# Performance work log

Measured on AMD Instinct MI355X. Metric: run time of the kernel, lower is better.

## Reference

```python
import jax, jax.numpy as jnp
import numpy as np

NEG = -9e8

def _leaky(x):
    return jax.nn.leaky_relu(x, 0.01)

def _gru(x, h, wih, whh, bih, bhh):
    # torch.nn.GRUCell math
    gi = x @ wih.T + bih
    gh = h @ whh.T + bhh
    ir, iz, inn = jnp.split(gi, 3, axis=-1)
    hr, hz, hn = jnp.split(gh, 3, axis=-1)
    r = jax.nn.sigmoid(ir + hr)
    z = jax.nn.sigmoid(iz + hz)
    n = jnp.tanh(inn + r * hn)
    return (1.0 - z) * n + z * h

def _gather(feat, idx):
    # feat [B,S,F], idx [B,S,K] -> [B,S,K,F]; -1 wraps to last row, masked later (same as torch)
    return jax.vmap(lambda f, i: f[i])(feat, idx)

def setup_inputs() -> dict:
    key = jax.random.key(0)
    ks = jax.random.split(key, 32)
    B, S, K, F_in, E, R = 32, 512, 21, 26, 256, 3
    amino_list = jax.random.uniform(ks[0], (B, S, F_in), dtype=jnp.float32)
    idx = jax.random.randint(ks[1], (B, S, K), 0, S, dtype=jnp.int32)
    pad = jax.random.uniform(ks[2], (B, S, K)) < 0.3
    amino_degree_list = jnp.where(pad, jnp.int32(-1), idx)
    # variable sequence lengths for mask
    lens = jax.random.randint(ks[3], (B,), S // 2, S + 1)
    amino_mask = (jnp.arange(S)[None, :] < lens[:, None]).astype(jnp.float32)
    s = 0.05
    d = dict(
        amino_list=amino_list,
        amino_degree_list=amino_degree_list,
        amino_mask=amino_mask,
        emb_W=jax.random.normal(ks[4], (E, F_in)) * s,
        emb_b=jax.random.normal(ks[5], (E,)) * s,
        neigh_W=jax.random.normal(ks[6], (E, F_in)) * s,
        neigh_b=jax.random.normal(ks[7], (E,)) * s,
        align_W=jax.random.normal(ks[8], (R, 1, 2 * E)) * s,
        align_b=jax.random.normal(ks[9], (R, 1)) * s,
        attend_W=jax.random.normal(ks[10], (R, E, E)) * s,
        attend_b=jax.random.normal(ks[11], (R, E)) * s,
        gru_wih=jax.random.normal(ks[12], (R, 3 * E, E)) * s,
        gru_whh=jax.random.normal(ks[13], (R, 3 * E, E)) * s,
        gru_bih=jax.random.normal(ks[14], (R, 3 * E)) * s,
        gru_bhh=jax.random.normal(ks[15], (R, 3 * E)) * s,
        seq_align_W=jax.random.normal(ks[16], (1, 2 * E)) * s,
        seq_align_b=jax.random.normal(ks[17], (1,)) * s,
        seq_attend_W=jax.random.normal(ks[18], (E, E)) * s,
        seq_attend_b=jax.random.normal(ks[19], (E,)) * s,
        sgru_wih=jax.random.normal(ks[20], (3 * E, E)) * s,
        sgru_whh=jax.random.normal(ks[21], (3 * E, E)) * s,
        sgru_bih=jax.random.normal(ks[22], (3 * E,)) * s,
        sgru_bhh=jax.random.normal(ks[23], (3 * E,)) * s,
    )
    return d

RADIUS = 3
T_STEPS = 2

def reference(amino_list, amino_degree_list, amino_mask,
              emb_W, emb_b, neigh_W, neigh_b,
              align_W, align_b, attend_W, attend_b,
              gru_wih, gru_whh, gru_bih, gru_bhh,
              seq_align_W, seq_align_b, seq_attend_W, seq_attend_b,
              sgru_wih, sgru_whh, sgru_bih, sgru_bhh):
    B, S, _ = amino_list.shape
    E = emb_W.shape[0]
    K = amino_degree_list.shape[-1]

    mask3 = amino_mask[:, :, None]                       # [B,S,1]
    amino_feature = _leaky(amino_list @ emb_W.T + emb_b)  # [B,S,E]

    attend_mask = (amino_degree_list != -1).astype(jnp.float32)[..., None]   # [B,S,K,1]
    softmax_mask = jnp.where(amino_degree_list == -1, NEG, 0.0)[..., None]   # [B,S,K,1]

    # first radius step: neighbors from raw one-hot features via neighbor_fc
    neighbor = _gather(amino_list, amino_degree_list)                 # [B,S,K,F_in]
    neighbor_feature = _leaky(neighbor @ neigh_W.T + neigh_b)         # [B,S,K,E]

    h = amino_feature.reshape(B * S, E)
    activated = None
    for d in range(RADIUS):
        if d == 0:
            nbr = neighbor_feature
            cur = amino_feature
        else:
            nbr = _gather(activated, amino_degree_list)               # [B,S,K,E]
            cur = activated
        cur_exp = jnp.broadcast_to(cur[:, :, None, :], (B, S, K, E))
        feat_align = jnp.concatenate([cur_exp, nbr], axis=-1)         # [B,S,K,2E]
        score = _leaky(feat_align @ align_W[d].T + align_b[d]) + softmax_mask
        attw = jax.nn.softmax(score, axis=-2) * attend_mask           # [B,S,K,1]
        nbr_t = nbr @ attend_W[d].T + attend_b[d]                     # [B,S,K,E]
        context = jax.nn.elu(jnp.sum(attw * nbr_t, axis=-2))          # [B,S,E]
        h = _gru(context.reshape(B * S, E), h, gru_wih[d], gru_whh[d], gru_bih[d], gru_bhh[d])
        activated = jax.nn.relu(h.reshape(B, S, E))

    seq_feature = jnp.sum(activated * mask3, axis=-2)                 # [B,E]
    act_mol = jax.nn.relu(seq_feature)
    seq_softmax_mask = jnp.where(mask3 == 0.0, NEG, 0.0)              # [B,S,1]

    act_seq = act_mol
    for _ in range(T_STEPS):
        mol_exp = jnp.broadcast_to(act_mol[:, None, :], (B, S, E))
        sa = jnp.concatenate([mol_exp, activated], axis=-1)           # [B,S,2E]
        score = _leaky(sa @ seq_align_W.T + seq_align_b) + seq_softmax_mask
        w = jax.nn.softmax(score, axis=-2) * mask3                    # [B,S,1]
        feat_t = activated @ seq_attend_W.T + seq_attend_b            # [B,S,E]
        seq_context = jax.nn.elu(jnp.sum(w * feat_t, axis=-2))        # [B,E]
        seq_feature = _gru(seq_context, seq_feature, sgru_wih, sgru_whh, sgru_bih, sgru_bhh)
        act_seq = jax.nn.relu(seq_feature)
    return act_seq
```

## Files before the change

### kernel.cpp

```cpp
#include <hip/hip_runtime.h>
#include <hip/hip_bf16.h>
#include <math.h>


#define NEGC (-9.0e8f)

typedef __attribute__((ext_vector_type(8))) short bf16x8;
typedef __attribute__((ext_vector_type(4))) float f32x4;

__device__ __forceinline__ ushort f2bf(float x) {
    union { float f; unsigned u; } v; v.f = x;
    unsigned r = v.u + 0x7FFF + ((v.u >> 16) & 1);
    return (ushort)(r >> 16);
}
__device__ __forceinline__ float bf2f(ushort u) {
    union { unsigned u; float f; } v; v.u = ((unsigned)u) << 16;
    return v.f;
}
__device__ __forceinline__ float sigm_fast(float x) {
    return 1.f / (1.f + __expf(-x));
}
__device__ __forceinline__ float tanh_fast(float x) {
    return 1.f - 2.f / (__expf(2.f * x) + 1.f);
}
__device__ __forceinline__ float elu_fast(float x) {
    return x > 0.f ? x : (__expf(x) - 1.f);
}

typedef const __attribute__((address_space(1))) void gvoid_t;
typedef __attribute__((address_space(3))) void lvoid_t;

__global__ __launch_bounds__(256) void cvt4_kernel(
    const float* __restrict__ s0, ushort* __restrict__ d0, int n0,
    const float* __restrict__ s1, ushort* __restrict__ d1, int n1,
    const float* __restrict__ s2, ushort* __restrict__ d2, int n2,
    const float* __restrict__ s3, ushort* __restrict__ d3, int n3)
{
    int i = blockIdx.x * 256 + threadIdx.x;
    const float* s; ushort* dst; int l;
    if (i < n0) { s = s0; dst = d0; l = i; }
    else if (i < n0 + n1) { s = s1; dst = d1; l = i - n0; }
    else if (i < n0 + n1 + n2) { s = s2; dst = d2; l = i - n0 - n1; }
    else if (i < n0 + n1 + n2 + n3) { s = s3; dst = d3; l = i - n0 - n1 - n2; }
    else return;
    float4 v = *reinterpret_cast<const float4*>(s + (size_t)l * 4);
    ushort4 o; o.x = f2bf(v.x); o.y = f2bf(v.y); o.z = f2bf(v.z); o.w = f2bf(v.w);
    *reinterpret_cast<ushort4*>(dst + (size_t)l * 4) = o;
}

__global__ __launch_bounds__(256) void gemm_dual_kernel(
    const ushort* __restrict__ A0, const ushort* __restrict__ W0,
    const float* __restrict__ b0, ushort* __restrict__ C0, int n0t,
    const ushort* __restrict__ A1, const ushort* __restrict__ W1,
    const float* __restrict__ b1, ushort* __restrict__ C1, int n1t,
    int K,
    const float* __restrict__ dw1, const float* __restrict__ dw2,
    float* __restrict__ dout1, float* __restrict__ dout2)
{
    __shared__ __align__(16) short As[128 * 32];
    __shared__ __align__(16) short Bs[128 * 32];
    int nwg = gridDim.x;
    int q = nwg >> 3;
    int flat = blockIdx.x;
    int sw = (flat & 7) * q + (flat >> 3);
    int tot = n0t + n1t;
    int bmi = sw / tot, bni = sw - bmi * tot;
    const ushort* A; const ushort* W; const float* bias; ushort* C; int N, bn;
    if (bni < n0t) { A = A0; W = W0; bias = b0; C = C0; N = n0t << 7; bn = bni << 7; }
    else { A = A1; W = W1; bias = b1; C = C1; N = n1t << 7; bn = (bni - n0t) << 7; }
    int bm = bmi << 7;

    int tid = threadIdx.x;
    int lane = tid & 63;
    int w = tid >> 6;
    int wr = w >> 1, wc = w & 1;
    bool dots = (dout1 != nullptr) && (bni == 0);

    f32x4 acc[4][4];
#pragma unroll
    for (int m = 0; m < 4; ++m)
#pragma unroll
        for (int n = 0; n < 4; ++n) acc[m][n] = (f32x4){0.f, 0.f, 0.f, 0.f};
    float p1 = 0.f, p2 = 0.f;

    for (int k0 = 0; k0 < K; k0 += 32) {
#pragma unroll
        for (int i = 0; i < 2; ++i) {
            int e = w * 1024 + i * 512 + lane * 8;
            int r = e >> 5, c = e & 31;
            const ushort* ga = A + (size_t)(bm + r) * K + (k0 + c);
            const ushort* gw = W + (size_t)(bn + r) * K + (k0 + c);
            __builtin_amdgcn_global_load_lds((gvoid_t*)ga, (lvoid_t*)&As[w * 1024 + i * 512], 16, 0, 0);
            __builtin_amdgcn_global_load_lds((gvoid_t*)gw, (lvoid_t*)&Bs[w * 1024 + i * 512], 16, 0, 0);
        }
        __syncthreads();
        bf16x8 af[4], bw[4];
        int ra = wr * 64 + (lane & 15);
        int rb = wc * 64 + (lane & 15);
        int kc = (lane >> 4) * 8;
#pragma unroll
        for (int m = 0; m < 4; ++m)
            af[m] = *reinterpret_cast<const bf16x8*>(&As[(ra + m * 16) * 32 + kc]);
#pragma unroll
        for (int n = 0; n < 4; ++n)
            bw[n] = *reinterpret_cast<const bf16x8*>(&Bs[(rb + n * 16) * 32 + kc]);
#pragma unroll
        for (int m = 0; m < 4; ++m)
#pragma unroll
            for (int n = 0; n < 4; ++n)
                acc[m][n] = __builtin_amdgcn_mfma_f32_16x16x32_bf16(af[m], bw[n], acc[m][n], 0, 0, 0);
        if (dots) {
            int drow = tid >> 1, kh = (tid & 1) << 4;
            const short* ar = &As[drow * 32 + kh];
#pragma unroll
            for (int c = 0; c < 16; ++c) {
                float av = bf2f((ushort)ar[c]);
                p1 = fmaf(av, dw1[k0 + kh + c], p1);
                if (dw2) p2 = fmaf(av, dw2[k0 + kh + c], p2);
            }
        }
        __syncthreads();
    }

    if (dots) {
        p1 += __shfl_xor(p1, 1);
        if (dw2) p2 += __shfl_xor(p2, 1);
        if ((tid & 1) == 0) {
            dout1[bm + (tid >> 1)] = p1;
            if (dw2) dout2[bm + (tid >> 1)] = p2;
        }
    }

    int cr0 = bm + wr * 64 + ((lane >> 4) * 4);
    int cc0 = bn + wc * 64 + (lane & 15);
#pragma unroll
    for (int n = 0; n < 4; ++n) {
        int col = cc0 + n * 16;
        float bv = bias[col];
#pragma unroll
        for (int m = 0; m < 4; ++m) {
            int row0 = cr0 + m * 16;
#pragma unroll
            for (int j = 0; j < 4; ++j) {
                float v = acc[m][n][j] + bv;
                C[(size_t)(row0 + j) * N + col] = f2bf(v);
            }
        }
    }
}

__global__ __launch_bounds__(256) void gru_fused_kernel(
    const ushort* __restrict__ ctx, const ushort* __restrict__ wih,
    const float* __restrict__ bih, const ushort* __restrict__ whh,
    const float* __restrict__ bhh,
    const ushort* __restrict__ h_in, ushort* __restrict__ h_out,
    ushort* __restrict__ act_bf,
    const float* __restrict__ mask, float* __restrict__ pool_part)
{
    __shared__ __align__(16) short lds[16384];
    int flat = blockIdx.x;
    int sw = (flat & 7) * 128 + (flat >> 3);
    int bmi = sw >> 2, ct = sw & 3;
    int bm = bmi << 6;
    int tid = threadIdx.x;
    int lane = tid & 63;
    int w = tid >> 6;
    int wr = w >> 1, wc = w & 1;

    f32x4 acc[6][2][2];
#pragma unroll
    for (int qq = 0; qq < 6; ++qq)
#pragma unroll
        for (int m = 0; m < 2; ++m)
#pragma unroll
            for (int n = 0; n < 2; ++n) acc[qq][m][n] = (f32x4){0.f, 0.f, 0.f, 0.f};

    int srow = tid >> 2, scol = (tid & 3) << 3;
    int ldst = (tid & 0xC0) * 8;
    for (int k0 = 0; k0 < 256; k0 += 32) {
        {
            const ushort* s0 = ctx  + (size_t)(bm + srow) * 256 + k0 + scol;
            const ushort* s1 = h_in + (size_t)(bm + srow) * 256 + k0 + scol;
            __builtin_amdgcn_global_load_lds((gvoid_t*)s0, (lvoid_t*)&lds[ldst], 16, 0, 0);
            __builtin_amdgcn_global_load_lds((gvoid_t*)s1, (lvoid_t*)&lds[2048 + ldst], 16, 0, 0);
#pragma unroll
            for (int qq = 0; qq < 6; ++qq) {
                const ushort* wb = (qq < 3) ? wih : whh;
                int slice = (qq < 3) ? qq : qq - 3;
                const ushort* sv = wb + (size_t)(slice * 256 + ct * 64 + srow) * 256 + k0 + scol;
                __builtin_amdgcn_global_load_lds((gvoid_t*)sv,
                    (lvoid_t*)&lds[(2 + qq) * 2048 + ldst], 16, 0, 0);
            }
        }
        __syncthreads();
        int rl = lane & 15;
        int kc = (lane >> 4) * 8;
        bf16x8 a_c[2], a_h[2];
#pragma unroll
        for (int m = 0; m < 2; ++m) {
            a_c[m] = *reinterpret_cast<const bf16x8*>(&lds[(wr * 32 + m * 16 + rl) * 32 + kc]);
            a_h[m] = *reinterpret_cast<const bf16x8*>(&lds[2048 + (wr * 32 + m * 16 + rl) * 32 + kc]);
        }
#pragma unroll
        for (int qq = 0; qq < 6; ++qq) {
            bf16x8 bw[2];
#pragma unroll
            for (int n = 0; n < 2; ++n)
                bw[n] = *reinterpret_cast<const bf16x8*>(
                    &lds[(2 + qq) * 2048 + (wc * 32 + n * 16 + rl) * 32 + kc]);
#pragma unroll
            for (int m = 0; m < 2; ++m)
#pragma unroll
                for (int n = 0; n < 2; ++n)
                    acc[qq][m][n] = __builtin_amdgcn_mfma_f32_16x16x32_bf16(
                        (qq < 3) ? a_c[m] : a_h[m], bw[n], acc[qq][m][n], 0, 0, 0);
        }
        __syncthreads();
    }

    int rl = lane & 15;
    int r0 = (lane >> 4) * 4;
    float mv[2][4];
    if (pool_part) {
        int b_ = bm >> 9;
        int sbase = bm & 511;
#pragma unroll
        for (int m = 0; m < 2; ++m)
#pragma unroll
            for (int j = 0; j < 4; ++j)
                mv[m][j] = mask[b_ * 512 + sbase + wr * 32 + m * 16 + r0 + j];
    }
    float pm[2] = {0.f, 0.f};

#pragma unroll
    for (int n = 0; n < 2; ++n) {
        int col = ct * 64 + wc * 32 + n * 16 + rl;
        float bir = bih[col], biz = bih[256 + col], bin = bih[512 + col];
        float bhr = bhh[col], bhz = bhh[256 + col], bhn = bhh[512 + col];
#pragma unroll
        for (int m = 0; m < 2; ++m) {
            int row0 = bm + wr * 32 + m * 16 + r0;
#pragma unroll
            for (int j = 0; j < 4; ++j) {
                size_t idx = (size_t)(row0 + j) * 256 + col;
                float r = sigm_fast(acc[0][m][n][j] + bir + acc[3][m][n][j] + bhr);
                float z = sigm_fast(acc[1][m][n][j] + biz + acc[4][m][n][j] + bhz);
                float nn = tanh_fast(acc[2][m][n][j] + bin + r * (acc[5][m][n][j] + bhn));
                float hold = bf2f(h_in[idx]);
                float hh = (1.f - z) * nn + z * hold;
                h_out[idx] = f2bf(hh);
                float a = fmaxf(hh, 0.f);
                act_bf[idx] = f2bf(a);
                if (pool_part) pm[n] = fmaf(a, mv[m][j], pm[n]);
            }
        }
    }

    if (pool_part) {
#pragma unroll
        for (int n = 0; n < 2; ++n) {
            float p = pm[n];
            p += __shfl_xor(p, 16);
            p += __shfl_xor(p, 32);
            if (lane < 16) {
                int b_ = bm >> 9;
                int sc = ((bm & 511) >> 5) + wr;
                int col = ct * 64 + wc * 32 + n * 16 + rl;
                pool_part[((size_t)b_ * 16 + sc) * 256 + col] = p;
            }
        }
    }
}

__global__ __launch_bounds__(256) void embed_kernel(
    const float* __restrict__ amino, const float* __restrict__ embW,
    const float* __restrict__ embB, const float* __restrict__ neighW,
    const float* __restrict__ neighB, const float* __restrict__ alignW,
    ushort* __restrict__ h_bf, ushort* __restrict__ nf_bf,
    float* __restrict__ ca, float* __restrict__ cb)
{
    const int FIN = 26, FPAD = 28, ROWS = 64;
    __shared__ __align__(16) float xs[ROWS][FPAD];
    __shared__ float red1[ROWS][4];
    __shared__ float red2[ROWS][4];
    int tid = threadIdx.x;
    int lane = tid & 63, wv = tid >> 6;
    float wE[FPAD], wN[FPAD];
#pragma unroll
    for (int f = 0; f < FIN; ++f) {
        wE[f] = embW[tid * FIN + f];
        wN[f] = neighW[tid * FIN + f];
    }
    wE[26] = wE[27] = wN[26] = wN[27] = 0.f;
    float b1 = embB[tid], b2 = neighB[tid];
    float w1t = alignW[tid], w2t = alignW[256 + tid];
    int row0 = blockIdx.x * ROWS;
    for (int idx = tid; idx < ROWS * FPAD; idx += 256) {
        int r = idx / FPAD, f = idx - r * FPAD;
        xs[r][f] = (f < FIN) ? amino[(size_t)(row0 + r) * FIN + f] : 0.f;
    }
    __syncthreads();
    for (int r = 0; r < ROWS; ++r) {
        const float4* x4 = reinterpret_cast<const float4*>(xs[r]);
        float a = b1, c = b2;
#pragma unroll
        for (int q = 0; q < 7; ++q) {
            float4 x = x4[q];
            a = fmaf(x.x, wE[4 * q], a);     c = fmaf(x.x, wN[4 * q], c);
            a = fmaf(x.y, wE[4 * q + 1], a); c = fmaf(x.y, wN[4 * q + 1], c);
            a = fmaf(x.z, wE[4 * q + 2], a); c = fmaf(x.z, wN[4 * q + 2], c);
            a = fmaf(x.w, wE[4 * q + 3], a); c = fmaf(x.w, wN[4 * q + 3], c);
        }
        a = a > 0.f ? a : 0.01f * a;
        c = c > 0.f ? c : 0.01f * c;
        size_t idx = (size_t)(row0 + r) * 256 + tid;
        h_bf[idx] = f2bf(a);
        nf_bf[idx] = f2bf(c);
        float p1 = a * w1t, p2 = c * w2t;
#pragma unroll
        for (int off = 32; off > 0; off >>= 1) {
            p1 += __shfl_down(p1, off);
            p2 += __shfl_down(p2, off);
        }
        if (lane == 0) { red1[r][wv] = p1; red2[r][wv] = p2; }
    }
    __syncthreads();
    if (tid < ROWS)
        ca[row0 + tid] = red1[tid][0] + red1[tid][1] + red1[tid][2] + red1[tid][3];
    else if (tid < 2 * ROWS) {
        int r = tid - ROWS;
        cb[row0 + r] = red2[r][0] + red2[r][1] + red2[r][2] + red2[r][3];
    }
}

__global__ __launch_bounds__(256) void attn_kernel(
    const int* __restrict__ deg, const float* __restrict__ ca,
    const float* __restrict__ cbrow, const ushort* __restrict__ act_t,
    const float* __restrict__ alignB, int d,
    ushort* __restrict__ context_bf, int S)
{
    const int KNB = 21;
    int raw = blockIdx.x;
    int bid = (raw & 7) * 512 + (raw >> 3);
    int bs0 = bid * 4;
    int b = bs0 >> 9;
    int tid = threadIdx.x;
    int wv = tid >> 6, lane = tid & 63;
    int bs = bs0 + wv;
    __shared__ float ss[4][KNB];
    __shared__ int   sj[4][KNB];
    if (lane < KNB) {
        int j = deg[bs * KNB + lane];
        float cbv = (j >= 0) ? cbrow[b * S + j] : 0.f;
        float sc = ca[bs] + cbv + alignB[d];
        sc = sc > 0.f ? sc : 0.01f * sc;
        if (j < 0) sc += NEGC;
        sj[wv][lane] = j;
        ss[wv][lane] = sc;
    }
    __syncthreads();
    float mx = -3.4e38f;
#pragma unroll
    for (int k = 0; k < KNB; ++k) mx = fmaxf(mx, ss[wv][k]);
    float se[KNB];
    float sum = 0.f;
#pragma unroll
    for (int k = 0; k < KNB; ++k) { se[k] = __expf(ss[wv][k] - mx); sum += se[k]; }
    float inv = 1.f / sum;
    const ushort* base = act_t + (size_t)b * S * 256 + lane * 4;
    float a0 = 0.f, a1 = 0.f, a2 = 0.f, a3 = 0.f;
#pragma unroll
    for (int k = 0; k < KNB; ++k) {
        int j = sj[wv][k];
        if (j >= 0) {
            ushort4 v = *reinterpret_cast<const ushort4*>(base + (size_t)j * 256);
            float wk = se[k];
            a0 = fmaf(wk, bf2f(v.x), a0);
            a1 = fmaf(wk, bf2f(v.y), a1);
            a2 = fmaf(wk, bf2f(v.z), a2);
            a3 = fmaf(wk, bf2f(v.w), a3);
        }
    }
    ushort4 o;
    o.x = f2bf(elu_fast(a0 * inv));
    o.y = f2bf(elu_fast(a1 * inv));
    o.z = f2bf(elu_fast(a2 * inv));
    o.w = f2bf(elu_fast(a3 * inv));
    *reinterpret_cast<ushort4*>(&context_bf[(size_t)bs * 256 + lane * 4]) = o;
}

__global__ __launch_bounds__(256) void seqpool_sm_kernel(
    const float* __restrict__ partial, const float* __restrict__ saW,
    const float* __restrict__ praw, const float* __restrict__ sab,
    const float* __restrict__ mask,
    float* __restrict__ seqfeat, float* __restrict__ wout, int NC, int S)
{
    int b = blockIdx.x, tid = threadIdx.x;
    int lane = tid & 63, wv = tid >> 6;
    __shared__ float red[4];
    __shared__ float sw[512];
    __shared__ float r1[4], r2[4];
    __shared__ float smd;
    float acc = 0.f;
    for (int c = 0; c < NC; ++c)
        acc += partial[((size_t)b * NC + c) * 256 + tid];
    seqfeat[b * 256 + tid] = acc;
    float am = fmaxf(acc, 0.f);
    float p = am * saW[tid];
#pragma unroll
    for (int off = 32; off > 0; off >>= 1) p += __shfl_down(p, off);
    if (lane == 0) red[wv] = p;
    __syncthreads();
    if (tid == 0) smd = red[0] + red[1] + red[2] + red[3];
    __syncthreads();
    float md = smd, sb = sab[0];
    float lm = -3.4e38f;
    for (int s = tid; s < S; s += 256) {
        float sc = md + praw[b * S + s] + sb;
        sc = sc > 0.f ? sc : 0.01f * sc;
        if (mask[b * S + s] == 0.f) sc += NEGC;
        sw[s] = sc;
        lm = fmaxf(lm, sc);
    }
#pragma unroll
    for (int off = 32; off > 0; off >>= 1) lm = fmaxf(lm, __shfl_down(lm, off));
    if (lane == 0) r1[wv] = lm;
    __syncthreads();
    float mx = fmaxf(fmaxf(r1[0], r1[1]), fmaxf(r1[2], r1[3]));
    float ls = 0.f;
    for (int s = tid; s < S; s += 256) {
        float e = __expf(sw[s] - mx);
        sw[s] = e * mask[b * S + s];
        ls += e;
    }
#pragma unroll
    for (int off = 32; off > 0; off >>= 1) ls += __shfl_down(ls, off);
    if (lane == 0) r2[wv] = ls;
    __syncthreads();
    float inv = 1.f / (r2[0] + r2[1] + r2[2] + r2[3]);
    for (int s = tid; s < S; s += 256)
        wout[b * S + s] = sw[s] * inv;
}

__global__ __launch_bounds__(256) void seqctx_partial_kernel(
    const float* __restrict__ w, const ushort* __restrict__ feat,
    float* __restrict__ partial, int S, int CH)
{
    int bc = blockIdx.x;
    int NC = S / CH;
    int b = bc / NC, c = bc - b * NC;
    int tid = threadIdx.x;
    int s0 = c * CH;
    const ushort* fb = feat + ((size_t)b * S + s0) * 256;
    const float* wb = w + b * S + s0;
    float acc = 0.f;
    for (int s = 0; s < CH; ++s)
        acc = fmaf(wb[s], bf2f(fb[(size_t)s * 256 + tid]), acc);
    partial[(size_t)bc * 256 + tid] = acc;
}

__global__ __launch_bounds__(256) void seqctx_combine_kernel(
    const float* __restrict__ partial, float* __restrict__ sctx, int NC)
{
    int b = blockIdx.x, tid = threadIdx.x;
    float acc = 0.f;
    for (int c = 0; c < NC; ++c)
        acc += partial[((size_t)b * NC + c) * 256 + tid];
    sctx[b * 256 + tid] = elu_fast(acc);
}

__global__ __launch_bounds__(256) void sgru_mm_kernel(
    const float* __restrict__ x, const float* __restrict__ hseq,
    const float* __restrict__ wih, const float* __restrict__ whh,
    const float* __restrict__ bih, const float* __restrict__ bhh,
    float* __restrict__ g, int full)
{
    int per_b = full ? 1536 : 768;
    int o = blockIdx.x * 4 + (threadIdx.x >> 6);
    int lane = threadIdx.x & 63;
    int b = o / per_b;
    int j = o - b * per_b;
    if (!full) j += 768;
    const float* src; const float* w; const float* bp; int jj;
    if (j < 768) { src = x + b * 256; w = wih; bp = bih; jj = j; }
    else         { src = hseq + b * 256; w = whh; bp = bhh; jj = j - 768; }
    float p = 0.f;
#pragma unroll
    for (int i = 0; i < 4; ++i) {
        int idx = lane + 64 * i;
        p = fmaf(src[idx], w[(size_t)jj * 256 + idx], p);
    }
#pragma unroll
    for (int off = 32; off > 0; off >>= 1) p += __shfl_down(p, off);
    if (lane == 0) g[b * 1536 + j] = p + bp[jj];
}

__global__ __launch_bounds__(256) void sgru_gate_kernel(
    const float* __restrict__ g, float* __restrict__ hseq, float* __restrict__ out)
{
    int b = blockIdx.x, e = threadIdx.x;
    const float* gr = g + b * 1536;
    float r = sigm_fast(gr[e] + gr[768 + e]);
    float z = sigm_fast(gr[256 + e] + gr[1024 + e]);
    float n = tanh_fast(gr[512 + e] + r * gr[1280 + e]);
    float hv = hseq[b * 256 + e];
    float hn = (1.f - z) * n + z * hv;
    hseq[b * 256 + e] = hn;
    out[b * 256 + e] = fmaxf(hn, 0.f);
}

extern "C" void kernel_launch(void* const* d_in, const int* in_sizes, int n_in,
                              void* d_out, int out_size, void* d_ws, size_t ws_size,
                              hipStream_t stream)
{
    const float* amino   = (const float*)d_in[0];
    const int*   deg     = (const int*)  d_in[1];
    const float* mask    = (const float*)d_in[2];
    const float* embW    = (const float*)d_in[3];
    const float* embB    = (const float*)d_in[4];
    const float* neighW  = (const float*)d_in[5];
    const float* neighB  = (const float*)d_in[6];
    const float* alignW  = (const float*)d_in[7];
    const float* alignB  = (const float*)d_in[8];
    const float* attendW = (const float*)d_in[9];
    const float* attendB = (const float*)d_in[10];
    const float* gruWih  = (const float*)d_in[11];
    const float* gruWhh  = (const float*)d_in[12];
    const float* gruBih  = (const float*)d_in[13];
    const float* gruBhh  = (const float*)d_in[14];
    const float* saW     = (const float*)d_in[15];
    const float* saB     = (const float*)d_in[16];
    const float* seqAttW = (const float*)d_in[17];
    const float* seqAttB = (const float*)d_in[18];
    const float* sWih    = (const float*)d_in[19];
    const float* sWhh    = (const float*)d_in[20];
    const float* sBih    = (const float*)d_in[21];
    const float* sBhh    = (const float*)d_in[22];
    float* out = (float*)d_out;

    const int B = 32, S = 512;
    const int BS = B * S;
    const size_t N1 = (size_t)BS * 256;

    ushort* hA     = (ushort*)d_ws;
    ushort* hB     = hA + N1;
    ushort* act_bf = hB + N1;
    ushort* nb_bf  = act_bf + N1;
    ushort* att_bf = nb_bf + N1;
    ushort* attW_bf = att_bf + N1;
    ushort* wih_bf  = attW_bf + 3 * 256 * 256;
    ushort* whh_bf  = wih_bf + 3 * 768 * 256;
    ushort* saW2_bf = whh_bf + 3 * 768 * 256;
    float* smalls = (float*)(saW2_bf + 256 * 256);
    float* ca   = smalls;
    float* cb   = ca + BS;
    float* scor = cb + BS;
    float* wbuf = scor + BS;
    float* seqf = wbuf + BS;
    float* sctx = seqf + B * 256;
    float* g    = sctx + B * 256;
    float* part = g + B * 1536;

    const int c0 = (3 * 256 * 256) / 4, c1 = (3 * 768 * 256) / 4,
              c2 = (3 * 768 * 256) / 4, c3 = (256 * 256) / 4;
    cvt4_kernel<<<(c0 + c1 + c2 + c3 + 255) / 256, 256, 0, stream>>>(
        attendW, attW_bf, c0, gruWih, wih_bf, c1, gruWhh, whh_bf, c2, seqAttW, saW2_bf, c3);

    embed_kernel<<<BS / 64, 256, 0, stream>>>(amino, embW, embB, neighW, neighB, alignW,
                                              hA, nb_bf, ca, cb);

    for (int d = 0; d < 3; ++d) {
        const ushort* nbr_bf = (d == 0) ? nb_bf : act_bf;
        const ushort* h_in  = (d & 1) ? hB : hA;
        ushort*       h_out = (d & 1) ? hA : hB;
        gemm_dual_kernel<<<128 * 2, 256, 0, stream>>>(
            nbr_bf, attW_bf + d * 256 * 256, attendB + d * 256, att_bf, 2,
            (const ushort*)nullptr, (const ushort*)nullptr, (const float*)nullptr,
            (ushort*)nullptr, 0, 256,
            d == 0 ? (const float*)nullptr : alignW + d * 512,
            d == 0 ? (const float*)nullptr : alignW + d * 512 + 256,
            d == 0 ? (float*)nullptr : ca,
            d == 0 ? (float*)nullptr : cb);
        attn_kernel<<<BS / 4, 256, 0, stream>>>(deg, ca, cb, att_bf, alignB, d, nb_bf, S);
        gru_fused_kernel<<<1024, 256, 0, stream>>>(
            nb_bf, wih_bf + d * 768 * 256, gruBih + d * 768,
            whh_bf + d * 768 * 256, gruBhh + d * 768, h_in, h_out, act_bf,
            (d == 2) ? mask : (const float*)nullptr,
            (d == 2) ? part : (float*)nullptr);
    }

    gemm_dual_kernel<<<128 * 2, 256, 0, stream>>>(
        act_bf, saW2_bf, seqAttB, att_bf, 2,
        (const ushort*)nullptr, (const ushort*)nullptr, (const float*)nullptr,
        (ushort*)nullptr, 0, 256,
        saW + 256, (const float*)nullptr, scor, (float*)nullptr);
    seqpool_sm_kernel<<<B, 256, 0, stream>>>(part, saW, scor, saB, mask, seqf, wbuf, 16, S);
    seqctx_partial_kernel<<<B * 16, 256, 0, stream>>>(wbuf, att_bf, part, S, 32);
    seqctx_combine_kernel<<<B, 256, 0, stream>>>(part, sctx, 16);

    sgru_mm_kernel<<<B * 1536 / 4, 256, 0, stream>>>(sctx, seqf, sWih, sWhh, sBih, sBhh, g, 1);
    sgru_gate_kernel<<<B, 256, 0, stream>>>(g, seqf, out);
    sgru_mm_kernel<<<B * 768 / 4, 256, 0, stream>>>(sctx, seqf, sWih, sWhh, sBih, sBhh, g, 0);
    sgru_gate_kernel<<<B, 256, 0, stream>>>(g, seqf, out);
}
```

Before: 284.3 us.

## Reassociate sequence attention: pool activations before projection, fuse score dot into GRU

Removes the full [B*S,256]x[256,256] sequence-attend GEMM by computing the weighted pool of activations first and then projecting the pooled vector per batch, using the sum of weights times bias. The per-row alignment score dot product is fused into the last GRU epilogue as partial sums across 8 column slices, which the softmax kernel then adds up. This drops one large GEMM launch and its bf16 output traffic, and trades them for a small per-batch matvec kernel plus extra shuffle reductions in the GRU epilogue. Weight conversion for the sequence attend matrix is also dropped.

```diff
diff --git a/kernel.cpp b/kernel.cpp
--- a/kernel.cpp
+++ b/kernel.cpp
@@ -30,18 +30,16 @@
 typedef const __attribute__((address_space(1))) void gvoid_t;
 typedef __attribute__((address_space(3))) void lvoid_t;
 
-__global__ __launch_bounds__(256) void cvt4_kernel(
+__global__ __launch_bounds__(256) void cvt3_kernel(
     const float* __restrict__ s0, ushort* __restrict__ d0, int n0,
     const float* __restrict__ s1, ushort* __restrict__ d1, int n1,
-    const float* __restrict__ s2, ushort* __restrict__ d2, int n2,
-    const float* __restrict__ s3, ushort* __restrict__ d3, int n3)
+    const float* __restrict__ s2, ushort* __restrict__ d2, int n2)
 {
     int i = blockIdx.x * 256 + threadIdx.x;
     const float* s; ushort* dst; int l;
     if (i < n0) { s = s0; dst = d0; l = i; }
     else if (i < n0 + n1) { s = s1; dst = d1; l = i - n0; }
     else if (i < n0 + n1 + n2) { s = s2; dst = d2; l = i - n0 - n1; }
-    else if (i < n0 + n1 + n2 + n3) { s = s3; dst = d3; l = i - n0 - n1 - n2; }
     else return;
     float4 v = *reinterpret_cast<const float4*>(s + (size_t)l * 4);
     ushort4 o; o.x = f2bf(v.x); o.y = f2bf(v.y); o.z = f2bf(v.z); o.w = f2bf(v.w);
@@ -51,8 +49,6 @@
 __global__ __launch_bounds__(256) void gemm_dual_kernel(
     const ushort* __restrict__ A0, const ushort* __restrict__ W0,
     const float* __restrict__ b0, ushort* __restrict__ C0, int n0t,
-    const ushort* __restrict__ A1, const ushort* __restrict__ W1,
-    const float* __restrict__ b1, ushort* __restrict__ C1, int n1t,
     int K,
     const float* __restrict__ dw1, const float* __restrict__ dw2,
     float* __restrict__ dout1, float* __restrict__ dout2)
@@ -63,11 +59,9 @@
     int q = nwg >> 3;
     int flat = blockIdx.x;
     int sw = (flat & 7) * q + (flat >> 3);
-    int tot = n0t + n1t;
-    int bmi = sw / tot, bni = sw - bmi * tot;
-    const ushort* A; const ushort* W; const float* bias; ushort* C; int N, bn;
-    if (bni < n0t) { A = A0; W = W0; bias = b0; C = C0; N = n0t << 7; bn = bni << 7; }
-    else { A = A1; W = W1; bias = b1; C = C1; N = n1t << 7; bn = (bni - n0t) << 7; }
+    int bmi = sw / n0t, bni = sw - bmi * n0t;
+    const ushort* A = A0; const ushort* W = W0; const float* bias = b0;
+    ushort* C = C0; int N = n0t << 7; int bn = bni << 7;
     int bm = bmi << 7;
 
     int tid = threadIdx.x;
@@ -116,7 +110,7 @@
             for (int c = 0; c < 16; ++c) {
                 float av = bf2f((ushort)ar[c]);
                 p1 = fmaf(av, dw1[k0 + kh + c], p1);
-                if (dw2) p2 = fmaf(av, dw2[k0 + kh + c], p2);
+                p2 = fmaf(av, dw2[k0 + kh + c], p2);
             }
         }
         __syncthreads();
@@ -124,10 +118,10 @@
 
     if (dots) {
         p1 += __shfl_xor(p1, 1);
-        if (dw2) p2 += __shfl_xor(p2, 1);
+        p2 += __shfl_xor(p2, 1);
         if ((tid & 1) == 0) {
             dout1[bm + (tid >> 1)] = p1;
-            if (dw2) dout2[bm + (tid >> 1)] = p2;
+            dout2[bm + (tid >> 1)] = p2;
         }
     }
 
@@ -155,7 +149,8 @@
     const float* __restrict__ bhh,
     const ushort* __restrict__ h_in, ushort* __restrict__ h_out,
     ushort* __restrict__ act_bf,
-    const float* __restrict__ mask, float* __restrict__ pool_part)
+    const float* __restrict__ mask, float* __restrict__ pool_part,
+    const float* __restrict__ dsw, float* __restrict__ scor_part, int BS)
 {
     __shared__ __align__(16) short lds[16384];
     int flat = blockIdx.x;
@@ -221,6 +216,7 @@
     int rl = lane & 15;
     int r0 = (lane >> 4) * 4;
     float mv[2][4];
+    float dswv[2];
     if (pool_part) {
         int b_ = bm >> 9;
         int sbase = bm & 511;
@@ -229,8 +225,12 @@
 #pragma unroll
             for (int j = 0; j < 4; ++j)
                 mv[m][j] = mask[b_ * 512 + sbase + wr * 32 + m * 16 + r0 + j];
+#pragma unroll
+        for (int n = 0; n < 2; ++n)
+            dswv[n] = dsw[ct * 64 + wc * 32 + n * 16 + rl];
     }
     float pm[2] = {0.f, 0.f};
+    float ps[2][4] = {{0.f, 0.f, 0.f, 0.f}, {0.f, 0.f, 0.f, 0.f}};
 
 #pragma unroll
     for (int n = 0; n < 2; ++n) {
@@ -251,7 +251,10 @@
                 h_out[idx] = f2bf(hh);
                 float a = fmaxf(hh, 0.f);
                 act_bf[idx] = f2bf(a);
-                if (pool_part) pm[n] = fmaf(a, mv[m][j], pm[n]);
+                if (pool_part) {
+                    pm[n] = fmaf(a, mv[m][j], pm[n]);
+                    ps[m][j] = fmaf(a, dswv[n], ps[m][j]);
+                }
             }
         }
     }
@@ -269,6 +272,20 @@
                 pool_part[((size_t)b_ * 16 + sc) * 256 + col] = p;
             }
         }
+#pragma unroll
+        for (int m = 0; m < 2; ++m)
+#pragma unroll
+            for (int j = 0; j < 4; ++j) {
+                float p = ps[m][j];
+                p += __shfl_xor(p, 1);
+                p += __shfl_xor(p, 2);
+                p += __shfl_xor(p, 4);
+                p += __shfl_xor(p, 8);
+                if (rl == 0) {
+                    int row = bm + wr * 32 + m * 16 + r0 + j;
+                    scor_part[(size_t)(ct * 2 + wc) * BS + row] = p;
+                }
+            }
     }
 }
 
@@ -391,15 +408,16 @@
 
 __global__ __launch_bounds__(256) void seqpool_sm_kernel(
     const float* __restrict__ partial, const float* __restrict__ saW,
-    const float* __restrict__ praw, const float* __restrict__ sab,
+    const float* __restrict__ scor_part, const float* __restrict__ sab,
     const float* __restrict__ mask,
-    float* __restrict__ seqfeat, float* __restrict__ wout, int NC, int S)
+    float* __restrict__ seqfeat, float* __restrict__ wout,
+    float* __restrict__ wsumb, int NC, int S, int BS)
 {
     int b = blockIdx.x, tid = threadIdx.x;
     int lane = tid & 63, wv = tid >> 6;
     __shared__ float red[4];
     __shared__ float sw[512];
-    __shared__ float r1[4], r2[4];
+    __shared__ float r1[4], r2[4], r3[4];
     __shared__ float smd;
     float acc = 0.f;
     for (int c = 0; c < NC; ++c)
@@ -416,9 +434,13 @@
     float md = smd, sb = sab[0];
     float lm = -3.4e38f;
     for (int s = tid; s < S; s += 256) {
-        float sc = md + praw[b * S + s] + sb;
+        int row = b * S + s;
+        float praw = 0.f;
+#pragma unroll
+        for (int sl = 0; sl < 8; ++sl) praw += scor_part[(size_t)sl * BS + row];
+        float sc = md + praw + sb;
         sc = sc > 0.f ? sc : 0.01f * sc;
-        if (mask[b * S + s] == 0.f) sc += NEGC;
+        if (mask[row] == 0.f) sc += NEGC;
         sw[s] = sc;
         lm = fmaxf(lm, sc);
     }
@@ -427,46 +449,74 @@
     if (lane == 0) r1[wv] = lm;
     __syncthreads();
     float mx = fmaxf(fmaxf(r1[0], r1[1]), fmaxf(r1[2], r1[3]));
-    float ls = 0.f;
+    float ls = 0.f, ms = 0.f;
     for (int s = tid; s < S; s += 256) {
         float e = __expf(sw[s] - mx);
-        sw[s] = e * mask[b * S + s];
+        float em = e * mask[b * S + s];
+        sw[s] = em;
         ls += e;
-    }
-#pragma unroll
-    for (int off = 32; off > 0; off >>= 1) ls += __shfl_down(ls, off);
-    if (lane == 0) r2[wv] = ls;
+        ms += em;
+    }
+#pragma unroll
+    for (int off = 32; off > 0; off >>= 1) {
+        ls += __shfl_down(ls, off);
+        ms += __shfl_down(ms, off);
+    }
+    if (lane == 0) { r2[wv] = ls; r3[wv] = ms; }
     __syncthreads();
     float inv = 1.f / (r2[0] + r2[1] + r2[2] + r2[3]);
+    if (tid == 0) wsumb[b] = (r3[0] + r3[1] + r3[2] + r3[3]) * inv;
     for (int s = tid; s < S; s += 256)
         wout[b * S + s] = sw[s] * inv;
 }
 
-__global__ __launch_bounds__(256) void seqctx_partial_kernel(
-    const float* __restrict__ w, const ushort* __restrict__ feat,
-    float* __restrict__ partial, int S, int CH)
+__global__ __launch_bounds__(256) void wpool_kernel(
+    const float* __restrict__ w, const ushort* __restrict__ act,
+    float* __restrict__ vpart, int S, int CH)
 {
     int bc = blockIdx.x;
     int NC = S / CH;
     int b = bc / NC, c = bc - b * NC;
     int tid = threadIdx.x;
     int s0 = c * CH;
-    const ushort* fb = feat + ((size_t)b * S + s0) * 256;
+    const ushort* ab = act + ((size_t)b * S + s0) * 256;
     const float* wb = w + b * S + s0;
     float acc = 0.f;
     for (int s = 0; s < CH; ++s)
-        acc = fmaf(wb[s], bf2f(fb[(size_t)s * 256 + tid]), acc);
-    partial[(size_t)bc * 256 + tid] = acc;
-}
-
-__global__ __launch_bounds__(256) void seqctx_combine_kernel(
-    const float* __restrict__ partial, float* __restrict__ sctx, int NC)
+        acc = fmaf(wb[s], bf2f(ab[(size_t)s * 256 + tid]), acc);
+    vpart[(size_t)bc * 256 + tid] = acc;
+}
+
+__global__ __launch_bounds__(256) void combineV_kernel(
+    const float* __restrict__ vpart, float* __restrict__ V, int NC)
 {
     int b = blockIdx.x, tid = threadIdx.x;
     float acc = 0.f;
     for (int c = 0; c < NC; ++c)
-        acc += partial[((size_t)b * NC + c) * 256 + tid];
-    sctx[b * 256 + tid] = elu_fast(acc);
+        acc += vpart[((size_t)b * NC + c) * 256 + tid];
+    V[b * 256 + tid] = acc;
+}
+
+__global__ __launch_bounds__(256) void sctx_mm_kernel(
+    const float* __restrict__ V, const float* __restrict__ seqAttW,
+    const float* __restrict__ seqAttB, const float* __restrict__ wsumb,
+    float* __restrict__ sctx)
+{
+    int o = blockIdx.x * 4 + (threadIdx.x >> 6);
+    int lane = threadIdx.x & 63;
+    int b = o >> 8, col = o & 255;
+    const float* vb = V + b * 256;
+    const float* wr_ = seqAttW + (size_t)col * 256;
+    float p = 0.f;
+#pragma unroll
+    for (int i = 0; i < 4; ++i) {
+        int idx = lane + 64 * i;
+        p = fmaf(vb[idx], wr_[idx], p);
+    }
+#pragma unroll
+    for (int off = 32; off > 0; off >>= 1) p += __shfl_down(p, off);
+    if (lane == 0)
+        sctx[o] = elu_fast(p + wsumb[b] * seqAttB[col]);
 }
 
 __global__ __launch_bounds__(256) void sgru_mm_kernel(
@@ -550,21 +600,23 @@
     ushort* attW_bf = att_bf + N1;
     ushort* wih_bf  = attW_bf + 3 * 256 * 256;
     ushort* whh_bf  = wih_bf + 3 * 768 * 256;
-    ushort* saW2_bf = whh_bf + 3 * 768 * 256;
-    float* smalls = (float*)(saW2_bf + 256 * 256);
-    float* ca   = smalls;
-    float* cb   = ca + BS;
-    float* scor = cb + BS;
-    float* wbuf = scor + BS;
-    float* seqf = wbuf + BS;
-    float* sctx = seqf + B * 256;
-    float* g    = sctx + B * 256;
-    float* part = g + B * 1536;
+    float* smalls = (float*)(whh_bf + 3 * 768 * 256);
+    float* ca    = smalls;
+    float* cb    = ca + BS;
+    float* wbuf  = cb + BS;
+    float* scorp = wbuf + BS;
+    float* seqf  = scorp + 8 * BS;
+    float* sctx  = seqf + B * 256;
+    float* V     = sctx + B * 256;
+    float* wsumb = V + B * 256;
+    float* g     = wsumb + 256;
+    float* part  = g + B * 1536;
+    float* vpart = part + B * 16 * 256;
 
     const int c0 = (3 * 256 * 256) / 4, c1 = (3 * 768 * 256) / 4,
-              c2 = (3 * 768 * 256) / 4, c3 = (256 * 256) / 4;
-    cvt4_kernel<<<(c0 + c1 + c2 + c3 + 255) / 256, 256, 0, stream>>>(
-        attendW, attW_bf, c0, gruWih, wih_bf, c1, gruWhh, whh_bf, c2, seqAttW, saW2_bf, c3);
+              c2 = (3 * 768 * 256) / 4;
+    cvt3_kernel<<<(c0 + c1 + c2 + 255) / 256, 256, 0, stream>>>(
+        attendW, attW_bf, c0, gruWih, wih_bf, c1, gruWhh, whh_bf, c2);
 
     embed_kernel<<<BS / 64, 256, 0, stream>>>(amino, embW, embB, neighW, neighB, alignW,
                                               hA, nb_bf, ca, cb);
@@ -574,9 +626,7 @@
         const ushort* h_in  = (d & 1) ? hB : hA;
         ushort*       h_out = (d & 1) ? hA : hB;
         gemm_dual_kernel<<<128 * 2, 256, 0, stream>>>(
-            nbr_bf, attW_bf + d * 256 * 256, attendB + d * 256, att_bf, 2,
-            (const ushort*)nullptr, (const ushort*)nullptr, (const float*)nullptr,
-            (ushort*)nullptr, 0, 256,
+            nbr_bf, attW_bf + d * 256 * 256, attendB + d * 256, att_bf, 2, 256,
             d == 0 ? (const float*)nullptr : alignW + d * 512,
             d == 0 ? (const float*)nullptr : alignW + d * 512 + 256,
             d == 0 ? (float*)nullptr : ca,
@@ -586,17 +636,15 @@
             nb_bf, wih_bf + d * 768 * 256, gruBih + d * 768,
             whh_bf + d * 768 * 256, gruBhh + d * 768, h_in, h_out, act_bf,
             (d == 2) ? mask : (const float*)nullptr,
-            (d == 2) ? part : (float*)nullptr);
-    }
-
-    gemm_dual_kernel<<<128 * 2, 256, 0, stream>>>(
-        act_bf, saW2_bf, seqAttB, att_bf, 2,
-        (const ushort*)nullptr, (const ushort*)nullptr, (const float*)nullptr,
-        (ushort*)nullptr, 0, 256,
-        saW + 256, (const float*)nullptr, scor, (float*)nullptr);
-    seqpool_sm_kernel<<<B, 256, 0, stream>>>(part, saW, scor, saB, mask, seqf, wbuf, 16, S);
-    seqctx_partial_kernel<<<B * 16, 256, 0, stream>>>(wbuf, att_bf, part, S, 32);
-    seqctx_combine_kernel<<<B, 256, 0, stream>>>(part, sctx, 16);
+            (d == 2) ? part : (float*)nullptr,
+            saW + 256, scorp, BS);
+    }
+
+    seqpool_sm_kernel<<<B, 256, 0, stream>>>(part, saW, scorp, saB, mask,
+                                             seqf, wbuf, wsumb, 16, S, BS);
+    wpool_kernel<<<B * 16, 256, 0, stream>>>(wbuf, act_bf, vpart, S, 32);
+    combineV_kernel<<<B, 256, 0, stream>>>(vpart, V, 16);
+    sctx_mm_kernel<<<B * 256 / 4, 256, 0, stream>>>(V, seqAttW, seqAttB, wsumb, sctx);
 
     sgru_mm_kernel<<<B * 1536 / 4, 256, 0, stream>>>(sctx, seqf, sWih, sWhh, sBih, sBhh, g, 1);
     sgru_gate_kernel<<<B, 256, 0, stream>>>(g, seqf, out);
```

Result: slower. 307.1 us (+8.0%).
